# Kernel optimization log

Measured on AMD Instinct MI355X. Metric: run time of the kernel, lower is better.

## Reference

```python
import jax, jax.numpy as jnp
import numpy as np

H = 512; W = 512; PH = 16; PW = 16; Q = 3; JITTER = 1e-06
NH = H // PH; NW = W // PW; P = NH * NW
B = 64


def setup_inputs() -> dict:
    key = jax.random.key(0)
    k0, k1, k2, k3, k4 = jax.random.split(key, 5)
    x = jax.random.normal(k0, (B, H, W), dtype=jnp.float32)
    logits = jax.random.normal(k1, (P, Q), dtype=jnp.float32)
    mu = jax.random.normal(k2, (P, Q, 2), dtype=jnp.float32) * 0.3
    sigma = jnp.exp(jax.random.normal(k3, (P, Q, 2), dtype=jnp.float32) * 0.3)
    bias = jax.random.normal(k4, (P, PH, PW), dtype=jnp.float32)
    return {"x": x, "logits": logits, "mu": mu, "sigma": sigma, "bias": bias}


def _make_S(logits, mu, sigma):
    # logits: (P,Q), mu/sigma: (P,Q,2) -> S: (P,PH,PW)
    w = jax.nn.softmax(logits, axis=-1)            # (P,Q)
    fy = jnp.fft.fftfreq(PH).astype(jnp.float32)   # (PH,)
    fx = jnp.fft.fftfreq(PW).astype(jnp.float32)   # (PW,)
    mu_y = mu[..., 0][:, :, None, None]            # (P,Q,1,1)
    mu_x = mu[..., 1][:, :, None, None]
    sg_y = sigma[..., 0][:, :, None, None]
    sg_x = sigma[..., 1][:, :, None, None]
    fy_b = fy[None, None, :, None]                 # (1,1,PH,1)
    fx_b = fx[None, None, None, :]                 # (1,1,1,PW)
    g1 = jnp.exp(-0.5 * (((fy_b - mu_y) / sg_y) ** 2 + ((fx_b - mu_x) / sg_x) ** 2))
    g2 = jnp.exp(-0.5 * (((fy_b + mu_y) / sg_y) ** 2 + ((fx_b + mu_x) / sg_x) ** 2))
    # weighted sum over mixture components Q
    S = jnp.einsum('pq,pqhw->phw', w, g1 + g2) + JITTER
    return S


def reference(x, logits, mu, sigma, bias):
    # x: (B,H,W) -> (B,H,W)
    S = _make_S(logits, mu, sigma)                                  # (P,PH,PW)
    x_p = x.reshape(B, NH, PH, NW, PW)
    x_p = x_p.transpose(1, 3, 0, 2, 4).reshape(P, B, PH, PW)        # (P,B,PH,PW)
    Xf = jnp.fft.fftn(x_p, axes=(-2, -1))                           # complex64
    y_p = jnp.fft.ifftn(Xf * S[:, None, :, :], axes=(-2, -1)).real  # (P,B,PH,PW)
    y_p = y_p + bias[:, None, :, :]
    y = y_p.reshape(NH, NW, B, PH, PW)
    y = y.transpose(2, 0, 3, 1, 4).reshape(B, H, W)
    return y
```

## Files before the change

kernel.cpp:

```cpp
#include <hip/hip_runtime.h>
#include <math.h>

#define HH 512
#define WW 512
#define QQ 3

#define SROW 260
#define YROW 104

__device__ __forceinline__ void wfence() { asm volatile("" ::: "memory"); }

template <int SGN, int T>
__device__ __forceinline__ void bfly(float& ar, float& ai, float& br, float& bi) {
  float tr, ti;
  if constexpr (T == 0) {
    tr = br;
    ti = bi;
  } else if constexpr (T == 4) {
    if constexpr (SGN > 0) { tr = bi;  ti = -br; }
    else                   { tr = -bi; ti = br;  }
  } else if constexpr (T == 2) {
    constexpr float c = 0.70710678118654752440f;
    if constexpr (SGN > 0) { tr = c * (br + bi); ti = c * (bi - br); }
    else                   { tr = c * (br - bi); ti = c * (bi + br); }
  } else if constexpr (T == 6) {
    constexpr float c = 0.70710678118654752440f;
    if constexpr (SGN > 0) { tr = c * (bi - br);  ti = -c * (br + bi); }
    else                   { tr = -c * (br + bi); ti = c * (br - bi);  }
  } else {
    constexpr float c1 = 0.92387953251128675613f;
    constexpr float s1 = 0.38268343236508977173f;
    constexpr float wr = (T == 1) ? c1 : (T == 3) ? s1 : (T == 5) ? -s1 : -c1;
    constexpr float wi0 = (T == 1) ? -s1 : (T == 3) ? -c1 : (T == 5) ? -c1 : -s1;
    constexpr float wi = (SGN > 0) ? wi0 : -wi0;
    tr = br * wr - bi * wi;
    ti = br * wi + bi * wr;
  }
  br = ar - tr;
  bi = ai - ti;
  ar = ar + tr;
  ai = ai + ti;
}

template <int SGN>
__device__ __forceinline__ void fft16(float re[16], float im[16]) {
#define SW_(a, b)                              \
  { float t = re[a]; re[a] = re[b]; re[b] = t; \
    t = im[a]; im[a] = im[b]; im[b] = t; }
  SW_(1, 8) SW_(2, 4) SW_(3, 12) SW_(5, 10) SW_(7, 14) SW_(11, 13)
#undef SW_
#define BF_(a, b, T) bfly<SGN, T>(re[a], im[a], re[b], im[b]);
  BF_(0, 1, 0) BF_(2, 3, 0) BF_(4, 5, 0) BF_(6, 7, 0)
  BF_(8, 9, 0) BF_(10, 11, 0) BF_(12, 13, 0) BF_(14, 15, 0)
  BF_(0, 2, 0) BF_(1, 3, 4) BF_(4, 6, 0) BF_(5, 7, 4)
  BF_(8, 10, 0) BF_(9, 11, 4) BF_(12, 14, 0) BF_(13, 15, 4)
  BF_(0, 4, 0) BF_(1, 5, 2) BF_(2, 6, 4) BF_(3, 7, 6)
  BF_(8, 12, 0) BF_(9, 13, 2) BF_(10, 14, 4) BF_(11, 15, 6)
  BF_(0, 8, 0) BF_(1, 9, 1) BF_(2, 10, 2) BF_(3, 11, 3)
  BF_(4, 12, 4) BF_(5, 13, 5) BF_(6, 14, 6) BF_(7, 15, 7)
#undef BF_
}

__global__ __launch_bounds__(256) void psm_kernel(
    const float* __restrict__ x, const float* __restrict__ logits,
    const float* __restrict__ mu, const float* __restrict__ sigma,
    const float* __restrict__ bias, float* __restrict__ out) {
  __shared__ float xs[16 * SROW];
  __shared__ float zim[16 * SROW];
  __shared__ float ytab[16 * YROW];

  const int tid = threadIdx.x;
  const int bid = blockIdx.x;
  const int half = bid & 1;
  const int nh = (bid >> 1) & 31;
  const int b = bid >> 6;

  const size_t xbase =
      (size_t)b * (HH * WW) + (size_t)(nh * 16) * WW + (size_t)(half * 256);

  const int w = tid >> 6;
  const int colv = tid & 63;

  float4 v0, v1, v2, v3;
  {
    const float* src = x + xbase + (size_t)(colv * 4);
    v0 = *(const float4*)(src + (size_t)((0 * 4 + w) * WW));
    v1 = *(const float4*)(src + (size_t)((1 * 4 + w) * WW));
    v2 = *(const float4*)(src + (size_t)((2 * 4 + w) * WW));
    v3 = *(const float4*)(src + (size_t)((3 * 4 + w) * WW));
  }

  const int nwl = tid >> 4;
  const int r = tid & 15;
  const int pg = nh * 32 + half * 16 + nwl;

  {
    const float fyr = (float)(r < 8 ? r : r - 16) * (1.0f / 16.0f);
#pragma unroll
    for (int m = 0; m < 6; ++m) {
      const int q = m >> 1;
      const float muy = mu[(pg * QQ + q) * 2 + 0];
      const float isy = 1.0f / sigma[(pg * QQ + q) * 2 + 0];
      const float d = ((m & 1) ? (fyr + muy) : (fyr - muy)) * isy;
      ytab[nwl * YROW + m * 16 + r] = __expf(-0.5f * d * d);
    }
  }

  {
    float* dst = &xs[colv * 4];
    *(float4*)(dst + (0 * 4 + w) * SROW) = v0;
    *(float4*)(dst + (1 * 4 + w) * SROW) = v1;
    *(float4*)(dst + (2 * 4 + w) * SROW) = v2;
    *(float4*)(dst + (3 * 4 + w) * SROW) = v3;
  }
  __syncthreads();

  float re[16], im[16];
  {
    const float* rb = &xs[r * SROW + nwl * 16];
#pragma unroll
    for (int c4 = 0; c4 < 4; ++c4) {
      const float4 t = *(const float4*)(rb + c4 * 4);
      re[c4 * 4 + 0] = t.x;
      re[c4 * 4 + 1] = t.y;
      re[c4 * 4 + 2] = t.z;
      re[c4 * 4 + 3] = t.w;
    }
  }
#pragma unroll
  for (int c = 0; c < 16; ++c) im[c] = 0.0f;
  fft16<1>(re, im);
  {
    float* rbr = &xs[r * SROW + nwl * 16];
    float* rbi = &zim[r * SROW + nwl * 16];
#pragma unroll
    for (int c4 = 0; c4 < 4; ++c4) {
      float4 a, bb;
      a.x = re[c4 * 4 + 0]; a.y = re[c4 * 4 + 1];
      a.z = re[c4 * 4 + 2]; a.w = re[c4 * 4 + 3];
      bb.x = im[c4 * 4 + 0]; bb.y = im[c4 * 4 + 1];
      bb.z = im[c4 * 4 + 2]; bb.w = im[c4 * 4 + 3];
      *(float4*)(rbr + c4 * 4) = a;
      *(float4*)(rbi + c4 * 4) = bb;
    }
  }
  wfence();

  float s[16];
  {
    const float fxk = (float)(r < 8 ? r : r - 16) * (1.0f / 16.0f);
    const float l0 = logits[pg * QQ + 0];
    const float l1 = logits[pg * QQ + 1];
    const float l2 = logits[pg * QQ + 2];
    const float lm = fmaxf(l0, fmaxf(l1, l2));
    const float e0 = __expf(l0 - lm);
    const float e1 = __expf(l1 - lm);
    const float e2 = __expf(l2 - lm);
    const float inv = (1.0f / 256.0f) / (e0 + e1 + e2);
    float ax[6];
#pragma unroll
    for (int m = 0; m < 6; ++m) {
      const int q = m >> 1;
      const float mux = mu[(pg * QQ + q) * 2 + 1];
      const float isx = 1.0f / sigma[(pg * QQ + q) * 2 + 1];
      const float d = ((m & 1) ? (fxk + mux) : (fxk - mux)) * isx;
      const float wqv = ((q == 0) ? e0 : (q == 1) ? e1 : e2) * inv;
      ax[m] = wqv * __expf(-0.5f * d * d);
    }
    const float* yt = &ytab[nwl * YROW];
#pragma unroll
    for (int j4 = 0; j4 < 4; ++j4) {
      const float4 a0 = *(const float4*)(yt + 0 * 16 + j4 * 4);
      const float4 a1 = *(const float4*)(yt + 1 * 16 + j4 * 4);
      const float4 a2 = *(const float4*)(yt + 2 * 16 + j4 * 4);
      const float4 a3 = *(const float4*)(yt + 3 * 16 + j4 * 4);
      const float4 a4 = *(const float4*)(yt + 4 * 16 + j4 * 4);
      const float4 a5 = *(const float4*)(yt + 5 * 16 + j4 * 4);
      s[j4 * 4 + 0] = a0.x * ax[0] + a1.x * ax[1] + a2.x * ax[2] +
                      a3.x * ax[3] + a4.x * ax[4] + a5.x * ax[5] + 3.90625e-9f;
      s[j4 * 4 + 1] = a0.y * ax[0] + a1.y * ax[1] + a2.y * ax[2] +
                      a3.y * ax[3] + a4.y * ax[4] + a5.y * ax[5] + 3.90625e-9f;
      s[j4 * 4 + 2] = a0.z * ax[0] + a1.z * ax[1] + a2.z * ax[2] +
                      a3.z * ax[3] + a4.z * ax[4] + a5.z * ax[5] + 3.90625e-9f;
      s[j4 * 4 + 3] = a0.w * ax[0] + a1.w * ax[1] + a2.w * ax[2] +
                      a3.w * ax[3] + a4.w * ax[4] + a5.w * ax[5] + 3.90625e-9f;
    }
  }
  {
    const float* cbr = &xs[nwl * 16 + r];
    const float* cbi = &zim[nwl * 16 + r];
#pragma unroll
    for (int j = 0; j < 16; ++j) {
      re[j] = cbr[j * SROW];
      im[j] = cbi[j * SROW];
    }
  }
  fft16<1>(re, im);
#pragma unroll
  for (int j = 0; j < 16; ++j) {
    re[j] *= s[j];
    im[j] *= s[j];
  }
  fft16<-1>(re, im);
  {
    float* cbr = &xs[nwl * 16 + r];
    float* cbi = &zim[nwl * 16 + r];
#pragma unroll
    for (int j = 0; j < 16; ++j) {
      cbr[j * SROW] = re[j];
      cbi[j * SROW] = im[j];
    }
  }
  wfence();

  {
    const float* rbr = &xs[r * SROW + nwl * 16];
    const float* rbi = &zim[r * SROW + nwl * 16];
#pragma unroll
    for (int c4 = 0; c4 < 4; ++c4) {
      const float4 t = *(const float4*)(rbr + c4 * 4);
      const float4 u = *(const float4*)(rbi + c4 * 4);
      re[c4 * 4 + 0] = t.x; re[c4 * 4 + 1] = t.y;
      re[c4 * 4 + 2] = t.z; re[c4 * 4 + 3] = t.w;
      im[c4 * 4 + 0] = u.x; im[c4 * 4 + 1] = u.y;
      im[c4 * 4 + 2] = u.z; im[c4 * 4 + 3] = u.w;
    }
  }
  fft16<-1>(re, im);
  {
    const float* brow = bias + (size_t)pg * 256 + (size_t)(r * 16);
    float* rbo = &zim[r * SROW + nwl * 16];
#pragma unroll
    for (int c4 = 0; c4 < 4; ++c4) {
      const float4 bv = *(const float4*)(brow + c4 * 4);
      float4 o;
      o.x = re[c4 * 4 + 0] + bv.x;
      o.y = re[c4 * 4 + 1] + bv.y;
      o.z = re[c4 * 4 + 2] + bv.z;
      o.w = re[c4 * 4 + 3] + bv.w;
      *(float4*)(rbo + c4 * 4) = o;
    }
  }
  __syncthreads();

  {
    float* dst = out + xbase + (size_t)(colv * 4);
    const float* srcl = &zim[colv * 4];
#pragma unroll
    for (int j = 0; j < 4; ++j) {
      const float4 t = *(const float4*)(srcl + (j * 4 + w) * SROW);
      *(float4*)(dst + (size_t)((j * 4 + w) * WW)) = t;
    }
  }
}

extern "C" void kernel_launch(void* const* d_in, const int* in_sizes, int n_in,
                              void* d_out, int out_size, void* d_ws,
                              size_t ws_size, hipStream_t stream) {
  (void)in_sizes;
  (void)n_in;
  (void)out_size;
  (void)d_ws;
  (void)ws_size;
  const float* x = (const float*)d_in[0];
  const float* logits = (const float*)d_in[1];
  const float* mu = (const float*)d_in[2];
  const float* sigma = (const float*)d_in[3];
  const float* bias = (const float*)d_in[4];
  float* out = (float*)d_out;

  psm_kernel<<<dim3(64 * 32 * 2), dim3(256), 0, stream>>>(x, logits, mu, sigma,
                                                          bias, out);
}
```

Measured before the change: 133.0 us.

## Pack two batch images into one complex FFT as real and imaginary parts

```diff
diff --git a/kernel.cpp b/kernel.cpp
--- a/kernel.cpp
+++ b/kernel.cpp
@@ -73,21 +73,27 @@
   const int bid = blockIdx.x;
   const int half = bid & 1;
   const int nh = (bid >> 1) & 31;
-  const int b = bid >> 6;
-
-  const size_t xbase =
-      (size_t)b * (HH * WW) + (size_t)(nh * 16) * WW + (size_t)(half * 256);
+  const int pr = bid >> 6;
+
+  const size_t xbaseA = (size_t)(2 * pr) * (HH * WW) +
+                        (size_t)(nh * 16) * WW + (size_t)(half * 256);
+  const size_t xbaseB = xbaseA + (size_t)(HH * WW);
 
   const int w = tid >> 6;
   const int colv = tid & 63;
 
-  float4 v0, v1, v2, v3;
-  {
-    const float* src = x + xbase + (size_t)(colv * 4);
-    v0 = *(const float4*)(src + (size_t)((0 * 4 + w) * WW));
-    v1 = *(const float4*)(src + (size_t)((1 * 4 + w) * WW));
-    v2 = *(const float4*)(src + (size_t)((2 * 4 + w) * WW));
-    v3 = *(const float4*)(src + (size_t)((3 * 4 + w) * WW));
+  float4 a0, a1, a2, a3, b0, b1, b2, b3;
+  {
+    const float* srcA = x + xbaseA + (size_t)(colv * 4);
+    const float* srcB = x + xbaseB + (size_t)(colv * 4);
+    a0 = *(const float4*)(srcA + (size_t)((0 * 4 + w) * WW));
+    a1 = *(const float4*)(srcA + (size_t)((1 * 4 + w) * WW));
+    a2 = *(const float4*)(srcA + (size_t)((2 * 4 + w) * WW));
+    a3 = *(const float4*)(srcA + (size_t)((3 * 4 + w) * WW));
+    b0 = *(const float4*)(srcB + (size_t)((0 * 4 + w) * WW));
+    b1 = *(const float4*)(srcB + (size_t)((1 * 4 + w) * WW));
+    b2 = *(const float4*)(srcB + (size_t)((2 * 4 + w) * WW));
+    b3 = *(const float4*)(srcB + (size_t)((3 * 4 + w) * WW));
   }
 
   const int nwl = tid >> 4;
@@ -107,28 +113,33 @@
   }
 
   {
-    float* dst = &xs[colv * 4];
-    *(float4*)(dst + (0 * 4 + w) * SROW) = v0;
-    *(float4*)(dst + (1 * 4 + w) * SROW) = v1;
-    *(float4*)(dst + (2 * 4 + w) * SROW) = v2;
-    *(float4*)(dst + (3 * 4 + w) * SROW) = v3;
+    float* dstA = &xs[colv * 4];
+    float* dstB = &zim[colv * 4];
+    *(float4*)(dstA + (0 * 4 + w) * SROW) = a0;
+    *(float4*)(dstA + (1 * 4 + w) * SROW) = a1;
+    *(float4*)(dstA + (2 * 4 + w) * SROW) = a2;
+    *(float4*)(dstA + (3 * 4 + w) * SROW) = a3;
+    *(float4*)(dstB + (0 * 4 + w) * SROW) = b0;
+    *(float4*)(dstB + (1 * 4 + w) * SROW) = b1;
+    *(float4*)(dstB + (2 * 4 + w) * SROW) = b2;
+    *(float4*)(dstB + (3 * 4 + w) * SROW) = b3;
   }
   __syncthreads();
 
   float re[16], im[16];
   {
-    const float* rb = &xs[r * SROW + nwl * 16];
-#pragma unroll
-    for (int c4 = 0; c4 < 4; ++c4) {
-      const float4 t = *(const float4*)(rb + c4 * 4);
-      re[c4 * 4 + 0] = t.x;
-      re[c4 * 4 + 1] = t.y;
-      re[c4 * 4 + 2] = t.z;
-      re[c4 * 4 + 3] = t.w;
-    }
-  }
-#pragma unroll
-  for (int c = 0; c < 16; ++c) im[c] = 0.0f;
+    const float* rbr = &xs[r * SROW + nwl * 16];
+    const float* rbi = &zim[r * SROW + nwl * 16];
+#pragma unroll
+    for (int c4 = 0; c4 < 4; ++c4) {
+      const float4 t = *(const float4*)(rbr + c4 * 4);
+      const float4 u = *(const float4*)(rbi + c4 * 4);
+      re[c4 * 4 + 0] = t.x; re[c4 * 4 + 1] = t.y;
+      re[c4 * 4 + 2] = t.z; re[c4 * 4 + 3] = t.w;
+      im[c4 * 4 + 0] = u.x; im[c4 * 4 + 1] = u.y;
+      im[c4 * 4 + 2] = u.z; im[c4 * 4 + 3] = u.w;
+    }
+  }
   fft16<1>(re, im);
   {
     float* rbr = &xs[r * SROW + nwl * 16];
@@ -170,20 +181,20 @@
     const float* yt = &ytab[nwl * YROW];
 #pragma unroll
     for (int j4 = 0; j4 < 4; ++j4) {
-      const float4 a0 = *(const float4*)(yt + 0 * 16 + j4 * 4);
-      const float4 a1 = *(const float4*)(yt + 1 * 16 + j4 * 4);
-      const float4 a2 = *(const float4*)(yt + 2 * 16 + j4 * 4);
-      const float4 a3 = *(const float4*)(yt + 3 * 16 + j4 * 4);
-      const float4 a4 = *(const float4*)(yt + 4 * 16 + j4 * 4);
-      const float4 a5 = *(const float4*)(yt + 5 * 16 + j4 * 4);
-      s[j4 * 4 + 0] = a0.x * ax[0] + a1.x * ax[1] + a2.x * ax[2] +
-                      a3.x * ax[3] + a4.x * ax[4] + a5.x * ax[5] + 3.90625e-9f;
-      s[j4 * 4 + 1] = a0.y * ax[0] + a1.y * ax[1] + a2.y * ax[2] +
-                      a3.y * ax[3] + a4.y * ax[4] + a5.y * ax[5] + 3.90625e-9f;
-      s[j4 * 4 + 2] = a0.z * ax[0] + a1.z * ax[1] + a2.z * ax[2] +
-                      a3.z * ax[3] + a4.z * ax[4] + a5.z * ax[5] + 3.90625e-9f;
-      s[j4 * 4 + 3] = a0.w * ax[0] + a1.w * ax[1] + a2.w * ax[2] +
-                      a3.w * ax[3] + a4.w * ax[4] + a5.w * ax[5] + 3.90625e-9f;
+      const float4 a0v = *(const float4*)(yt + 0 * 16 + j4 * 4);
+      const float4 a1v = *(const float4*)(yt + 1 * 16 + j4 * 4);
+      const float4 a2v = *(const float4*)(yt + 2 * 16 + j4 * 4);
+      const float4 a3v = *(const float4*)(yt + 3 * 16 + j4 * 4);
+      const float4 a4v = *(const float4*)(yt + 4 * 16 + j4 * 4);
+      const float4 a5v = *(const float4*)(yt + 5 * 16 + j4 * 4);
+      s[j4 * 4 + 0] = a0v.x * ax[0] + a1v.x * ax[1] + a2v.x * ax[2] +
+                      a3v.x * ax[3] + a4v.x * ax[4] + a5v.x * ax[5] + 3.90625e-9f;
+      s[j4 * 4 + 1] = a0v.y * ax[0] + a1v.y * ax[1] + a2v.y * ax[2] +
+                      a3v.y * ax[3] + a4v.y * ax[4] + a5v.y * ax[5] + 3.90625e-9f;
+      s[j4 * 4 + 2] = a0v.z * ax[0] + a1v.z * ax[1] + a2v.z * ax[2] +
+                      a3v.z * ax[3] + a4v.z * ax[4] + a5v.z * ax[5] + 3.90625e-9f;
+      s[j4 * 4 + 3] = a0v.w * ax[0] + a1v.w * ax[1] + a2v.w * ax[2] +
+                      a3v.w * ax[3] + a4v.w * ax[4] + a5v.w * ax[5] + 3.90625e-9f;
     }
   }
   {
@@ -229,27 +240,40 @@
   fft16<-1>(re, im);
   {
     const float* brow = bias + (size_t)pg * 256 + (size_t)(r * 16);
-    float* rbo = &zim[r * SROW + nwl * 16];
+    float* rba = &xs[r * SROW + nwl * 16];
+    float* rbb = &zim[r * SROW + nwl * 16];
 #pragma unroll
     for (int c4 = 0; c4 < 4; ++c4) {
       const float4 bv = *(const float4*)(brow + c4 * 4);
-      float4 o;
-      o.x = re[c4 * 4 + 0] + bv.x;
-      o.y = re[c4 * 4 + 1] + bv.y;
-      o.z = re[c4 * 4 + 2] + bv.z;
-      o.w = re[c4 * 4 + 3] + bv.w;
-      *(float4*)(rbo + c4 * 4) = o;
+      float4 oA, oB;
+      oA.x = re[c4 * 4 + 0] + bv.x;
+      oA.y = re[c4 * 4 + 1] + bv.y;
+      oA.z = re[c4 * 4 + 2] + bv.z;
+      oA.w = re[c4 * 4 + 3] + bv.w;
+      oB.x = im[c4 * 4 + 0] + bv.x;
+      oB.y = im[c4 * 4 + 1] + bv.y;
+      oB.z = im[c4 * 4 + 2] + bv.z;
+      oB.w = im[c4 * 4 + 3] + bv.w;
+      *(float4*)(rba + c4 * 4) = oA;
+      *(float4*)(rbb + c4 * 4) = oB;
     }
   }
   __syncthreads();
 
   {
-    float* dst = out + xbase + (size_t)(colv * 4);
-    const float* srcl = &zim[colv * 4];
+    float* dstA = out + xbaseA + (size_t)(colv * 4);
+    float* dstB = out + xbaseB + (size_t)(colv * 4);
+    const float* srcA = &xs[colv * 4];
+    const float* srcB = &zim[colv * 4];
 #pragma unroll
     for (int j = 0; j < 4; ++j) {
-      const float4 t = *(const float4*)(srcl + (j * 4 + w) * SROW);
-      *(float4*)(dst + (size_t)((j * 4 + w) * WW)) = t;
+      const float4 tA = *(const float4*)(srcA + (j * 4 + w) * SROW);
+      *(float4*)(dstA + (size_t)((j * 4 + w) * WW)) = tA;
+    }
+#pragma unroll
+    for (int j = 0; j < 4; ++j) {
+      const float4 tB = *(const float4*)(srcB + (j * 4 + w) * SROW);
+      *(float4*)(dstB + (size_t)((j * 4 + w) * WW)) = tB;
     }
   }
 }
@@ -269,6 +293,6 @@
   const float* bias = (const float*)d_in[4];
   float* out = (float*)d_out;
 
-  psm_kernel<<<dim3(64 * 32 * 2), dim3(256), 0, stream>>>(x, logits, mu, sigma,
+  psm_kernel<<<dim3(32 * 32 * 2), dim3(256), 0, stream>>>(x, logits, mu, sigma,
                                                           bias, out);
 }
```

Measured after the change: 123.9 us. -6.8%, faster.
